# Kernel optimization log

Measured on AMD Instinct MI355X. Metric: run time of the kernel, lower is better.

Reference implementation:

```python
import jax, jax.numpy as jnp
import numpy as np

C = 384       # channels
K = 20        # select_k
P = 96        # num_patches
B, N, H, W = 8, 16, 32, 32


def setup_inputs() -> dict:
    key = jax.random.key(0)
    k1, k2, k3 = jax.random.split(key, 3)
    feature = jax.random.normal(k1, (B, N, C, H, W), dtype=jnp.float32)
    dw_w = jax.random.normal(k2, (C, 1, 3, 3), dtype=jnp.float32) * 0.05  # depthwise kernel (OIHW, groups=C)
    dw_b = jnp.zeros((C,), dtype=jnp.float32)
    pw_w = jax.random.normal(k3, (1, C, 1, 1), dtype=jnp.float32) * 0.05  # pointwise kernel
    pw_b = jnp.zeros((1,), dtype=jnp.float32)
    return {"feature": feature, "dw_w": dw_w, "dw_b": dw_b, "pw_w": pw_w, "pw_b": pw_b}


def reference(feature, dw_w, dw_b, pw_w, pw_b):
    b, n, c, h, w = feature.shape
    bn = b * n
    x = feature.reshape(bn, c, h, w)
    # depthwise 3x3 conv (groups = c)
    x = jax.lax.conv_general_dilated(
        x, dw_w, window_strides=(1, 1), padding='SAME',
        feature_group_count=c, dimension_numbers=('NCHW', 'OIHW', 'NCHW')
    ) + dw_b[None, :, None, None]
    # pointwise 1x1 conv -> 1 channel
    x = jax.lax.conv_general_dilated(
        x, pw_w, window_strides=(1, 1), padding='SAME',
        dimension_numbers=('NCHW', 'OIHW', 'NCHW')
    ) + pw_b[None, :, None, None]
    score = jax.nn.sigmoid(x).reshape(bn, h * w)

    # top-k voted patches (descending, sorted -> matches torch.topk)
    vote_values, vote_indices = jax.lax.top_k(score, K)

    # boolean scatter mask of selected positions
    mask = jnp.zeros((bn, h * w), dtype=bool)
    mask = mask.at[jnp.arange(bn)[:, None], vote_indices].set(True)

    # unselected indices in ascending order per row (stable sort: False first)
    unselected = jnp.argsort(mask, axis=1, stable=True)[:, : h * w - K]

    # single random permutation shared across rows (torch.randperm + expand)
    num_remaining = P - K
    perm = jax.random.permutation(jax.random.key(42), h * w - K)[:num_remaining]
    random_remaining = unselected[:, perm]

    x_coords = vote_indices % w
    y_coords = vote_indices // w
    # NOTE: original module keeps only the first n rows of the b*n batch
    x_select = jnp.clip(x_coords[:n, :], 1, w - 1)
    y_select = jnp.clip(y_coords[:n, :], 1, h - 1)
    x_remain = jnp.clip((random_remaining % w)[:n, :], 1, w - 1)
    y_remain = jnp.clip((random_remaining // w)[:n, :], 1, h - 1)

    x_out = jnp.concatenate([x_select, x_remain], axis=1)  # [n, P]
    y_out = jnp.concatenate([y_select, y_remain], axis=1)  # [n, P]
    return (x_out, y_out)
```

## Files before the change

kernel.cpp:

```cpp
#include <hip/hip_runtime.h>
#include <cstdint>
#include <cstddef>
#include <algorithm>

#define NROW 16
#define CTOT 384
#define HW   1024
#define KSEL 20
#define PSEL 96
#define NREM 76
#define NUNSEL 1004

#define CPB   8
#define SPLIT (CTOT / CPB)

typedef unsigned long long u64;

struct Perm76 { int p[NREM]; };

__device__ __forceinline__ void conv_job(const float4* f6, const float* w9,
                                         int b, int c, float acc[4][4])
{
  #pragma unroll
  for (int m = 0; m < 6; ++m) {
    float4 f = f6[m];
    const bool dead = (b == 0 && m == 0) || (b == 7 && m == 5);
    if (dead) { f.x = 0.f; f.y = 0.f; f.z = 0.f; f.w = 0.f; }
    float L = __shfl_up(f.w, 1);
    float R = __shfl_down(f.x, 1);
    if (c == 0) L = 0.f;
    if (c == 7) R = 0.f;
    const float c6[6] = { L, f.x, f.y, f.z, f.w, R };
    #pragma unroll
    for (int j = 0; j < 4; ++j) {
      const int d = m - j;
      if (d >= 0 && d < 3) {
        #pragma unroll
        for (int k = 0; k < 4; ++k)
          acc[j][k] += c6[k]     * w9[3 * d]
                     + c6[k + 1] * w9[3 * d + 1]
                     + c6[k + 2] * w9[3 * d + 2];
      }
    }
  }
}

__global__ __launch_bounds__(256) void pv_conv(
    const float* __restrict__ feat, const float* __restrict__ dw_w,
    const float* __restrict__ pw_w, float* __restrict__ partial)
{
  __shared__ float red[4][HW];
  const int t = threadIdx.x;
  const int w = t >> 6, lane = t & 63;
  const int b = lane >> 3, c = lane & 7;
  const int r = blockIdx.x & (NROW - 1);
  const int s = blockIdx.x >> 4;
  const int chA = s * CPB + 2 * w;
  const float* baseA = feat + ((size_t)r * CTOT + chA) * HW;
  const float* baseB = baseA + HW;

  float4 fa[6], fb[6];
  #pragma unroll
  for (int m = 0; m < 6; ++m) {
    const int row = 4 * b + m - 1;
    const int rc = row < 0 ? 0 : (row > 31 ? 31 : row);
    fa[m] = *reinterpret_cast<const float4*>(baseA + rc * 32 + 4 * c);
  }
  #pragma unroll
  for (int m = 0; m < 6; ++m) {
    const int row = 4 * b + m - 1;
    const int rc = row < 0 ? 0 : (row > 31 ? 31 : row);
    fb[m] = *reinterpret_cast<const float4*>(baseB + rc * 32 + 4 * c);
  }

  float wA[9], wB[9];
  {
    const float pa = pw_w[chA], pb = pw_w[chA + 1];
    #pragma unroll
    for (int i = 0; i < 9; ++i) {
      wA[i] = dw_w[chA * 9 + i] * pa;
      wB[i] = dw_w[(chA + 1) * 9 + i] * pb;
    }
  }

  float acc[4][4];
  #pragma unroll
  for (int j = 0; j < 4; ++j)
    #pragma unroll
    for (int k = 0; k < 4; ++k) acc[j][k] = 0.f;

  conv_job(fa, wA, b, c, acc);
  conv_job(fb, wB, b, c, acc);

  #pragma unroll
  for (int j = 0; j < 4; ++j)
    *reinterpret_cast<float4*>(&red[w][(4 * b + j) * 32 + 4 * c]) =
        make_float4(acc[j][0], acc[j][1], acc[j][2], acc[j][3]);
  __syncthreads();

  float4 sum = make_float4(0.f, 0.f, 0.f, 0.f);
  #pragma unroll
  for (int g = 0; g < 4; ++g) {
    const float4 v = *reinterpret_cast<const float4*>(&red[g][4 * t]);
    sum.x += v.x; sum.y += v.y; sum.z += v.z; sum.w += v.w;
  }
  *reinterpret_cast<float4*>(partial + ((size_t)(r * SPLIT + s)) * HW + 4 * t) = sum;
}

__global__ __launch_bounds__(256) void pv_reduceTopk(
    const float* __restrict__ partial, u64* __restrict__ cand)
{
  __shared__ float red[8][128];
  __shared__ u64 keysh[128];
  const int r = blockIdx.x >> 3;
  const int q = blockIdx.x & 7;
  const int t = threadIdx.x;
  const int sg = t >> 5, l32 = t & 31;

  const float* bp = partial + ((size_t)(r * SPLIT + sg)) * HW + q * 128 + 4 * l32;
  float4 a = make_float4(0.f, 0.f, 0.f, 0.f);
  #pragma unroll
  for (int i = 0; i < 6; ++i) {
    const float4 v = *reinterpret_cast<const float4*>(bp + (size_t)(8 * i) * HW);
    a.x += v.x; a.y += v.y; a.z += v.z; a.w += v.w;
  }
  *reinterpret_cast<float4*>(&red[sg][4 * l32]) = a;
  __syncthreads();

  if (t < 128) {
    float sc = 0.f;
    #pragma unroll
    for (int g = 0; g < 8; ++g) sc += red[g][t];
    const uint32_t bb = __float_as_uint(sc);
    const uint32_t mm = (bb & 0x80000000u) ? ~bb : (bb | 0x80000000u);
    const int gpx = q * 128 + t;
    keysh[t] = ((u64)mm << 32) | (uint32_t)(1023 - gpx);
  }
  __syncthreads();
  if (t < 128) {
    const u64 my = keysh[t];
    int rank = 0;
    for (int j = 0; j < 128; ++j) rank += (keysh[j] > my);
    if (rank < KSEL) cand[((size_t)(r * 8 + q)) * KSEL + rank] = my;
  }
}

__global__ __launch_bounds__(256) void pv_selectB2(
    const u64* __restrict__ cand, int* __restrict__ out, Perm76 perm)
{
  __shared__ u64 keysh[8 * KSEL];
  __shared__ int votes[KSEL];
  __shared__ int maskv[HW];
  __shared__ int wsumS[4];
  __shared__ int unsel[NUNSEL];

  const int r = blockIdx.x;
  const int t = threadIdx.x;
  const int lane = t & 63, wv = t >> 6;

  if (t < 8 * KSEL) keysh[t] = cand[(size_t)r * 8 * KSEL + t];
  maskv[t] = 0; maskv[t + 256] = 0; maskv[t + 512] = 0; maskv[t + 768] = 0;
  __syncthreads();

  if (t < 8 * KSEL) {
    const u64 my = keysh[t];
    int rank = 0;
    for (int j = 0; j < 8 * KSEL; ++j) rank += (keysh[j] > my);
    if (rank < KSEL) votes[rank] = 1023 - (int)(my & 1023ull);
  }
  __syncthreads();

  if (t < KSEL) {
    const int idx = votes[t];
    maskv[idx] = 1;
    int xx = idx & 31, yy = idx >> 5;
    if (xx < 1) xx = 1;
    if (yy < 1) yy = 1;
    out[r * PSEL + t]               = xx;
    out[NROW * PSEL + r * PSEL + t] = yy;
  }
  __syncthreads();

  int cnt = 0;
  #pragma unroll
  for (int j = 0; j < 4; ++j) cnt += (maskv[t * 4 + j] == 0);
  int inc = cnt;
  #pragma unroll
  for (int dd = 1; dd < 64; dd <<= 1) {
    const int o = __shfl_up(inc, dd);
    if (lane >= dd) inc += o;
  }
  if (lane == 63) wsumS[wv] = inc;
  __syncthreads();
  int basep = 0;
  for (int i = 0; i < 4; ++i) if (i < wv) basep += wsumS[i];
  int pos = basep + inc - cnt;
  #pragma unroll
  for (int j = 0; j < 4; ++j) {
    const int i = t * 4 + j;
    if (!maskv[i]) unsel[pos++] = i;
  }
  __syncthreads();

  if (t < NREM) {
    const int u = unsel[perm.p[t]];
    int xx = u & 31, yy = u >> 5;
    if (xx < 1) xx = 1;
    if (yy < 1) yy = 1;
    out[r * PSEL + KSEL + t]               = xx;
    out[NROW * PSEL + r * PSEL + KSEL + t] = yy;
  }
}

static inline uint32_t rotl32(uint32_t v, uint32_t n) { return (v << n) | (v >> (32 - n)); }

static void tf2x32(uint32_t k0, uint32_t k1, uint32_t x0, uint32_t x1,
                   uint32_t* o0, uint32_t* o1)
{
  const uint32_t ks[3] = { k0, k1, k0 ^ k1 ^ 0x1BD11BDAu };
  static const uint32_t rot[2][4] = { {13, 15, 26, 6}, {17, 29, 16, 24} };
  x0 += ks[0]; x1 += ks[1];
  for (int i = 0; i < 5; ++i) {
    const uint32_t* rr = rot[i & 1];
    for (int j = 0; j < 4; ++j) { x0 += x1; x1 = rotl32(x1, rr[j]); x1 ^= x0; }
    x0 += ks[(i + 1) % 3];
    x1 += ks[(i + 2) % 3] + (uint32_t)(i + 1);
  }
  *o0 = x0; *o1 = x1;
}

static void compute_perm(int* perm_out)
{
  uint32_t bits[NUNSEL];
  uint32_t sk0, sk1;
  { uint32_t o0, o1; tf2x32(0u, 42u, 0u, 1u, &o0, &o1); sk0 = o0; sk1 = o1; }
  for (int i = 0; i < NUNSEL; ++i) {
    uint32_t o0, o1; tf2x32(sk0, sk1, 0u, (uint32_t)i, &o0, &o1);
    bits[i] = o0 ^ o1;
  }
  int idx[NUNSEL];
  for (int i = 0; i < NUNSEL; ++i) idx[i] = i;
  std::stable_sort(idx, idx + NUNSEL, [&](int a, int b) { return bits[a] < bits[b]; });
  for (int j = 0; j < NREM; ++j) perm_out[j] = idx[j];
}

extern "C" void kernel_launch(void* const* d_in, const int* in_sizes, int n_in,
                              void* d_out, int out_size, void* d_ws, size_t ws_size,
                              hipStream_t stream)
{
  (void)in_sizes; (void)n_in; (void)out_size; (void)ws_size;
  const float* feat = (const float*)d_in[0];
  const float* dw_w = (const float*)d_in[1];
  const float* pw_w = (const float*)d_in[3];
  int*   out     = (int*)d_out;
  float* partial = (float*)d_ws;
  u64*   cand    = (u64*)((char*)d_ws + (size_t)NROW * SPLIT * HW * sizeof(float));

  Perm76 perm;
  compute_perm(perm.p);

  pv_conv<<<NROW * SPLIT, 256, 0, stream>>>(feat, dw_w, pw_w, partial);
  pv_reduceTopk<<<128, 256, 0, stream>>>(partial, cand);
  pv_selectB2<<<NROW, 256, 0, stream>>>(cand, out, perm);
}
```

Baseline: 18.02 us.

## Halve channels per conv block and fuse partial reduction with top-k selection

```diff
diff --git a/kernel.cpp b/kernel.cpp
--- a/kernel.cpp
+++ b/kernel.cpp
@@ -11,7 +11,7 @@
 #define NREM 76
 #define NUNSEL 1004
 
-#define CPB   8
+#define CPB   4
 #define SPLIT (CTOT / CPB)
 
 typedef unsigned long long u64;
@@ -55,32 +55,22 @@
   const int b = lane >> 3, c = lane & 7;
   const int r = blockIdx.x & (NROW - 1);
   const int s = blockIdx.x >> 4;
-  const int chA = s * CPB + 2 * w;
-  const float* baseA = feat + ((size_t)r * CTOT + chA) * HW;
-  const float* baseB = baseA + HW;
-
-  float4 fa[6], fb[6];
+  const int ch = s * CPB + w;
+  const float* base = feat + ((size_t)r * CTOT + ch) * HW;
+
+  float4 f[6];
   #pragma unroll
   for (int m = 0; m < 6; ++m) {
     const int row = 4 * b + m - 1;
     const int rc = row < 0 ? 0 : (row > 31 ? 31 : row);
-    fa[m] = *reinterpret_cast<const float4*>(baseA + rc * 32 + 4 * c);
-  }
-  #pragma unroll
-  for (int m = 0; m < 6; ++m) {
-    const int row = 4 * b + m - 1;
-    const int rc = row < 0 ? 0 : (row > 31 ? 31 : row);
-    fb[m] = *reinterpret_cast<const float4*>(baseB + rc * 32 + 4 * c);
-  }
-
-  float wA[9], wB[9];
+    f[m] = *reinterpret_cast<const float4*>(base + rc * 32 + 4 * c);
+  }
+
+  float w9[9];
   {
-    const float pa = pw_w[chA], pb = pw_w[chA + 1];
-    #pragma unroll
-    for (int i = 0; i < 9; ++i) {
-      wA[i] = dw_w[chA * 9 + i] * pa;
-      wB[i] = dw_w[(chA + 1) * 9 + i] * pb;
-    }
+    const float pw = pw_w[ch];
+    #pragma unroll
+    for (int i = 0; i < 9; ++i) w9[i] = dw_w[ch * 9 + i] * pw;
   }
 
   float acc[4][4];
@@ -89,8 +79,7 @@
     #pragma unroll
     for (int k = 0; k < 4; ++k) acc[j][k] = 0.f;
 
-  conv_job(fa, wA, b, c, acc);
-  conv_job(fb, wB, b, c, acc);
+  conv_job(f, w9, b, c, acc);
 
   #pragma unroll
   for (int j = 0; j < 4; ++j)
@@ -107,48 +96,11 @@
   *reinterpret_cast<float4*>(partial + ((size_t)(r * SPLIT + s)) * HW + 4 * t) = sum;
 }
 
-__global__ __launch_bounds__(256) void pv_reduceTopk(
-    const float* __restrict__ partial, u64* __restrict__ cand)
-{
-  __shared__ float red[8][128];
-  __shared__ u64 keysh[128];
-  const int r = blockIdx.x >> 3;
-  const int q = blockIdx.x & 7;
-  const int t = threadIdx.x;
-  const int sg = t >> 5, l32 = t & 31;
-
-  const float* bp = partial + ((size_t)(r * SPLIT + sg)) * HW + q * 128 + 4 * l32;
-  float4 a = make_float4(0.f, 0.f, 0.f, 0.f);
-  #pragma unroll
-  for (int i = 0; i < 6; ++i) {
-    const float4 v = *reinterpret_cast<const float4*>(bp + (size_t)(8 * i) * HW);
-    a.x += v.x; a.y += v.y; a.z += v.z; a.w += v.w;
-  }
-  *reinterpret_cast<float4*>(&red[sg][4 * l32]) = a;
-  __syncthreads();
-
-  if (t < 128) {
-    float sc = 0.f;
-    #pragma unroll
-    for (int g = 0; g < 8; ++g) sc += red[g][t];
-    const uint32_t bb = __float_as_uint(sc);
-    const uint32_t mm = (bb & 0x80000000u) ? ~bb : (bb | 0x80000000u);
-    const int gpx = q * 128 + t;
-    keysh[t] = ((u64)mm << 32) | (uint32_t)(1023 - gpx);
-  }
-  __syncthreads();
-  if (t < 128) {
-    const u64 my = keysh[t];
-    int rank = 0;
-    for (int j = 0; j < 128; ++j) rank += (keysh[j] > my);
-    if (rank < KSEL) cand[((size_t)(r * 8 + q)) * KSEL + rank] = my;
-  }
-}
-
-__global__ __launch_bounds__(256) void pv_selectB2(
-    const u64* __restrict__ cand, int* __restrict__ out, Perm76 perm)
-{
-  __shared__ u64 keysh[8 * KSEL];
+__global__ __launch_bounds__(256) void pv_select(
+    const float* __restrict__ partial, int* __restrict__ out, Perm76 perm)
+{
+  __shared__ u64 keysh[HW];
+  __shared__ u64 cand[8 * KSEL];
   __shared__ int votes[KSEL];
   __shared__ int maskv[HW];
   __shared__ int wsumS[4];
@@ -158,14 +110,54 @@
   const int t = threadIdx.x;
   const int lane = t & 63, wv = t >> 6;
 
-  if (t < 8 * KSEL) keysh[t] = cand[(size_t)r * 8 * KSEL + t];
+  const float* bp = partial + (size_t)r * SPLIT * HW + 4 * t;
+  float4 A[8];
+  #pragma unroll
+  for (int i = 0; i < 8; ++i) A[i] = make_float4(0.f, 0.f, 0.f, 0.f);
+  for (int s = 0; s < SPLIT; s += 8) {
+    #pragma unroll
+    for (int i = 0; i < 8; ++i) {
+      const float4 v = *reinterpret_cast<const float4*>(bp + (size_t)(s + i) * HW);
+      A[i].x += v.x; A[i].y += v.y; A[i].z += v.z; A[i].w += v.w;
+    }
+  }
+  #pragma unroll
+  for (int i = 1; i < 8; ++i) {
+    A[0].x += A[i].x; A[0].y += A[i].y; A[0].z += A[i].z; A[0].w += A[i].w;
+  }
+
+  const float sv[4] = { A[0].x, A[0].y, A[0].z, A[0].w };
+  u64 key[4];
+  #pragma unroll
+  for (int q = 0; q < 4; ++q) {
+    const int i = 4 * t + q;
+    const uint32_t bb = __float_as_uint(sv[q]);
+    const uint32_t mm = (bb & 0x80000000u) ? ~bb : (bb | 0x80000000u);
+    key[q] = ((u64)mm << 32) | (uint32_t)(1023 - i);
+    keysh[i] = key[q];
+  }
   maskv[t] = 0; maskv[t + 256] = 0; maskv[t + 512] = 0; maskv[t + 768] = 0;
   __syncthreads();
 
+  {
+    const u64* sk = &keysh[(t >> 5) * 128];
+    int rk0 = 0, rk1 = 0, rk2 = 0, rk3 = 0;
+    for (int j = 0; j < 128; ++j) {
+      const u64 kj = sk[j];
+      rk0 += (kj > key[0]); rk1 += (kj > key[1]);
+      rk2 += (kj > key[2]); rk3 += (kj > key[3]);
+    }
+    const int rk[4] = { rk0, rk1, rk2, rk3 };
+    #pragma unroll
+    for (int q = 0; q < 4; ++q)
+      if (rk[q] < KSEL) cand[(t >> 5) * KSEL + rk[q]] = key[q];
+  }
+  __syncthreads();
+
   if (t < 8 * KSEL) {
-    const u64 my = keysh[t];
+    const u64 my = cand[t];
     int rank = 0;
-    for (int j = 0; j < 8 * KSEL; ++j) rank += (keysh[j] > my);
+    for (int j = 0; j < 8 * KSEL; ++j) rank += (cand[j] > my);
     if (rank < KSEL) votes[rank] = 1023 - (int)(my & 1023ull);
   }
   __syncthreads();
@@ -254,12 +246,10 @@
   const float* pw_w = (const float*)d_in[3];
   int*   out     = (int*)d_out;
   float* partial = (float*)d_ws;
-  u64*   cand    = (u64*)((char*)d_ws + (size_t)NROW * SPLIT * HW * sizeof(float));
 
   Perm76 perm;
   compute_perm(perm.p);
 
   pv_conv<<<NROW * SPLIT, 256, 0, stream>>>(feat, dw_w, pw_w, partial);
-  pv_reduceTopk<<<128, 256, 0, stream>>>(partial, cand);
-  pv_selectB2<<<NROW, 256, 0, stream>>>(cand, out, perm);
-}
+  pv_select<<<NROW, 256, 0, stream>>>(partial, out, perm);
+}
```

Measured after the change: 22.99 us. 1.28x slower.

## Fuse final top-k selection into reduce kernel via last-block ticket

Applied to the files above, without the earlier changes.

```diff
diff --git a/kernel.cpp b/kernel.cpp
--- a/kernel.cpp
+++ b/kernel.cpp
@@ -47,7 +47,8 @@
 
 __global__ __launch_bounds__(256) void pv_conv(
     const float* __restrict__ feat, const float* __restrict__ dw_w,
-    const float* __restrict__ pw_w, float* __restrict__ partial)
+    const float* __restrict__ pw_w, float* __restrict__ partial,
+    int* __restrict__ ticket)
 {
   __shared__ float red[4][HW];
   const int t = threadIdx.x;
@@ -55,6 +56,9 @@
   const int b = lane >> 3, c = lane & 7;
   const int r = blockIdx.x & (NROW - 1);
   const int s = blockIdx.x >> 4;
+
+  if (s == 0 && t == 0) ticket[r] = 0;
+
   const int chA = s * CPB + 2 * w;
   const float* baseA = feat + ((size_t)r * CTOT + chA) * HW;
   const float* baseB = baseA + HW;
@@ -107,11 +111,19 @@
   *reinterpret_cast<float4*>(partial + ((size_t)(r * SPLIT + s)) * HW + 4 * t) = sum;
 }
 
-__global__ __launch_bounds__(256) void pv_reduceTopk(
-    const float* __restrict__ partial, u64* __restrict__ cand)
+__global__ __launch_bounds__(256) void pv_reduceSelect(
+    const float* __restrict__ partial, u64* __restrict__ cand,
+    int* __restrict__ ticket, int* __restrict__ out, Perm76 perm)
 {
   __shared__ float red[8][128];
   __shared__ u64 keysh[128];
+  __shared__ u64 candL[8 * KSEL];
+  __shared__ int votes[KSEL];
+  __shared__ int maskv[HW];
+  __shared__ int wsumS[4];
+  __shared__ int unsel[NUNSEL];
+  __shared__ int isFinS;
+
   const int r = blockIdx.x >> 3;
   const int q = blockIdx.x & 7;
   const int t = threadIdx.x;
@@ -141,31 +153,23 @@
     const u64 my = keysh[t];
     int rank = 0;
     for (int j = 0; j < 128; ++j) rank += (keysh[j] > my);
-    if (rank < KSEL) cand[((size_t)(r * 8 + q)) * KSEL + rank] = my;
-  }
-}
-
-__global__ __launch_bounds__(256) void pv_selectB2(
-    const u64* __restrict__ cand, int* __restrict__ out, Perm76 perm)
-{
-  __shared__ u64 keysh[8 * KSEL];
-  __shared__ int votes[KSEL];
-  __shared__ int maskv[HW];
-  __shared__ int wsumS[4];
-  __shared__ int unsel[NUNSEL];
-
-  const int r = blockIdx.x;
-  const int t = threadIdx.x;
-  const int lane = t & 63, wv = t >> 6;
-
-  if (t < 8 * KSEL) keysh[t] = cand[(size_t)r * 8 * KSEL + t];
+    if (rank < KSEL)
+      atomicExch(&cand[((size_t)(r * 8 + q)) * KSEL + rank], my);
+  }
+  __syncthreads();
+
+  if (t == 0) isFinS = (atomicAdd(&ticket[r], 1) == 7);
+  __syncthreads();
+  if (!isFinS) return;
+
+  if (t < 8 * KSEL) candL[t] = atomicAdd(&cand[(size_t)r * 8 * KSEL + t], 0ull);
   maskv[t] = 0; maskv[t + 256] = 0; maskv[t + 512] = 0; maskv[t + 768] = 0;
   __syncthreads();
 
   if (t < 8 * KSEL) {
-    const u64 my = keysh[t];
+    const u64 my = candL[t];
     int rank = 0;
-    for (int j = 0; j < 8 * KSEL; ++j) rank += (keysh[j] > my);
+    for (int j = 0; j < 8 * KSEL; ++j) rank += (candL[j] > my);
     if (rank < KSEL) votes[rank] = 1023 - (int)(my & 1023ull);
   }
   __syncthreads();
@@ -181,6 +185,7 @@
   }
   __syncthreads();
 
+  const int lane = t & 63, wv = t >> 6;
   int cnt = 0;
   #pragma unroll
   for (int j = 0; j < 4; ++j) cnt += (maskv[t * 4 + j] == 0);
@@ -255,11 +260,11 @@
   int*   out     = (int*)d_out;
   float* partial = (float*)d_ws;
   u64*   cand    = (u64*)((char*)d_ws + (size_t)NROW * SPLIT * HW * sizeof(float));
+  int*   ticket  = (int*)(cand + (size_t)NROW * 8 * KSEL);
 
   Perm76 perm;
   compute_perm(perm.p);
 
-  pv_conv<<<NROW * SPLIT, 256, 0, stream>>>(feat, dw_w, pw_w, partial);
-  pv_reduceTopk<<<128, 256, 0, stream>>>(partial, cand);
-  pv_selectB2<<<NROW, 256, 0, stream>>>(cand, out, perm);
-}
+  pv_conv<<<NROW * SPLIT, 256, 0, stream>>>(feat, dw_w, pw_w, partial, ticket);
+  pv_reduceSelect<<<128, 256, 0, stream>>>(partial, cand, ticket, out, perm);
+}
```

Result: no change. 18.05 us (+0.2%).
